# Kernel optimization log

Measured on AMD Instinct MI355X. Metric: run time of the kernel, lower is better.

The kernel has to match this reference:

```python
import jax, jax.numpy as jnp
import numpy as np

N_EXPERTS = 8
D_IN = 2048
D_OUT = 2048
BATCH = 8192


def setup_inputs() -> dict:
    key = jax.random.key(0)
    k_x, k_w, k_b, k_a, k_m = jax.random.split(key, 5)
    xs = jax.random.normal(k_x, (BATCH, D_IN), dtype=jnp.float32)
    # Expert parameters: each submodule modeled as Linear(D_IN, D_OUT)
    W = jax.random.normal(k_w, (N_EXPERTS, D_IN, D_OUT), dtype=jnp.float32) / np.sqrt(D_IN)
    b = jax.random.normal(k_b, (N_EXPERTS, D_OUT), dtype=jnp.float32) * 0.01
    actions = jax.random.randint(k_a, (BATCH,), 0, N_EXPERTS, dtype=jnp.int32)
    mxs = jax.random.randint(k_m, (BATCH,), 0, N_EXPERTS, dtype=jnp.int32)  # pass-through metadata
    return {"xs": xs, "W": W, "b": b, "mxs": mxs, "actions": actions}


def reference(xs, W, b, mxs, actions):
    # Original: per-sample split, route sample i to submodule actions[i], concat.
    # Vectorized MoE dispatch-combine: compute all expert outputs, select by one-hot.
    onehot = jax.nn.one_hot(actions, W.shape[0], dtype=xs.dtype)  # [B, E]
    # y_all[b,e,f] = xs[b,:] @ W[e,:,:]; combine with one-hot selection, add routed bias.
    ys = jnp.einsum('be,bd,edf->bf', onehot, xs, W) + b[actions]  # [B, D_OUT]
    return (ys, mxs, actions)
```

## Files before the change

### kernel.cpp

```cpp
#include <hip/hip_runtime.h>
#include <hip/hip_bf16.h>
#include <stdint.h>

#define BATCH 8192
#define GROWS 9216
#define DIN   2048
#define DOUT  2048
#define NEXP  8
#define BM    128
#define BN    256
#define BK    32
#define NT    (DIN / BK)
#define NSLOT 72
#define BUFSZ 24576
#define BOFF  8192

typedef __attribute__((ext_vector_type(4))) float fx4;
typedef __attribute__((ext_vector_type(8))) short sx8;

__device__ __forceinline__ short f2b(float x){
  unsigned u = __float_as_uint(x);
  u = u + 0x7FFFu + ((u >> 16) & 1u);
  return (short)(u >> 16);
}

__device__ __forceinline__ void gload16(const void* g, void* l){
  __builtin_amdgcn_global_load_lds(
      (const __attribute__((address_space(1))) unsigned int*)g,
      (__attribute__((address_space(3))) unsigned int*)l, 16, 0, 0);
}

__global__ void prep_count(const int* __restrict__ actions, int* __restrict__ perm,
                           int* __restrict__ meta){
  __shared__ int cnt[NEXP];
  int t = threadIdx.x;
  if (t < NEXP) cnt[t] = 0;
  for (int i = t; i < GROWS; i += 1024) perm[i] = -1;
  __syncthreads();
  for (int i = t; i < BATCH; i += 1024) atomicAdd(&cnt[actions[i]], 1);
  __syncthreads();
  if (t == 0){
    int s = 0, slot = 0;
    for (int e = 0; e < NEXP; ++e){
      meta[e] = s;
      int ns = (cnt[e] + BM - 1) / BM;
      for (int q = 0; q < ns; ++q) meta[17 + slot++] = e;
      s += ns * BM;
    }
    meta[16] = slot;
    meta[15] = 0;
  }
}

__global__ void prep_scatter(const int* __restrict__ actions, const int* __restrict__ mxs,
                             int* __restrict__ perm, int* __restrict__ meta,
                             float* __restrict__ out){
  int i = blockIdx.x * 256 + threadIdx.x;
  if (i < BATCH){
    int e = actions[i];
    int p = atomicAdd(&meta[e], 1);
    perm[p] = i;
    out[(size_t)BATCH * DOUT + i]         = (float)mxs[i];
    out[(size_t)BATCH * DOUT + BATCH + i] = (float)actions[i];
  }
}

__global__ void gatherx_kernel(const float* __restrict__ xs, const int* __restrict__ perm,
                               short* __restrict__ xp){
  int i = blockIdx.x;
  int t = threadIdx.x;
  short v[8];
  int p = perm[i];
  if (p >= 0){
    const fx4* src = (const fx4*)(xs + (size_t)p * DIN + t * 8);
    fx4 a = src[0], b2 = src[1];
    v[0]=f2b(a.x); v[1]=f2b(a.y); v[2]=f2b(a.z); v[3]=f2b(a.w);
    v[4]=f2b(b2.x); v[5]=f2b(b2.y); v[6]=f2b(b2.z); v[7]=f2b(b2.w);
  } else {
#pragma unroll
    for (int j = 0; j < 8; ++j) v[j] = 0;
  }
  *(sx8*)(xp + (size_t)i * DIN + t * 8) = *(const sx8*)v;
}

__global__ void transw_kernel(const float* __restrict__ W, short* __restrict__ Wt){
  __shared__ float tile[64][69];
  int e  = blockIdx.z;
  int n0 = blockIdx.x * 64;
  int k0 = blockIdx.y * 64;
  const float* Wp = W + (size_t)e * DIN * DOUT + (size_t)k0 * DOUT + n0;
  int t = threadIdx.x;
#pragma unroll
  for (int it = 0; it < 4; ++it){
    int r = it * 16 + (t >> 4);
    int c = (t & 15) * 4;
    fx4 v = *(const fx4*)(Wp + (size_t)r * DOUT + c);
    tile[r][c] = v.x; tile[r][c+1] = v.y; tile[r][c+2] = v.z; tile[r][c+3] = v.w;
  }
  __syncthreads();
  int n  = t >> 2;
  int kc = (t & 3) * 16;
  short vv[16];
#pragma unroll
  for (int j = 0; j < 16; ++j) vv[j] = f2b(tile[kc + j][n]);
  short* dst = Wt + (size_t)e * DOUT * DIN + (size_t)(n0 + n) * DIN + k0 + kc;
  *(sx8*)dst       = *(const sx8*)vv;
  *(sx8*)(dst + 8) = *(const sx8*)(vv + 8);
}

__global__ __launch_bounds__(512, 4)
void moe_gemm_kernel(const short* __restrict__ xp, const short* __restrict__ Wt,
                     const float* __restrict__ bias, const int* __restrict__ perm,
                     int* __restrict__ meta, float* __restrict__ out){
  __shared__ char lds[3 * BUFSZ];
  __shared__ int s_item;

  int nitems = meta[16] * 8;

  int t    = threadIdx.x;
  int wid  = t >> 6;
  int l    = t & 63;
  int wm   = wid & 1;
  int wn   = wid >> 1;
  int lrow = l & 15;
  int lk   = l >> 4;

  int srow = ((t >> 3) << 1) | ((t >> 2) & 1);
  int schk = (t & 3) ^ ((t >> 3) & 3);
  int ldst = t * 16;

  int arow = wm * 64 + lrow;
  int aline = arow >> 1;
  int addrA = aline * 128 + (arow & 1) * 64 + ((lk ^ (aline & 3)) << 4);
  int brow = wn * 64 + lrow;
  int bline = brow >> 1;
  int addrB = BOFF + bline * 128 + (brow & 1) * 64 + ((lk ^ (bline & 3)) << 4);

  for (;;){
    if (t == 0) s_item = atomicAdd(&meta[15], 1);
    __syncthreads();
    int item = s_item;
    if (item >= nitems) break;

    int slot = item >> 3, nb = item & 7;
    int e      = meta[17 + slot];
    int m_base = slot * BM;
    int n0     = nb * BN;

    const char* ag  = (const char*)xp + ((size_t)(m_base + srow) * DIN + schk * 8) * 2;
    const char* bg0 = (const char*)Wt + (((size_t)e * DOUT + n0 + srow) * DIN + schk * 8) * 2;
    const char* bg1 = bg0 + (size_t)128 * DIN * 2;

#define STAGE(kt, BASE) do{ \
    gload16(ag  + (size_t)(kt) * 64, lds + (BASE) + ldst); \
    gload16(bg0 + (size_t)(kt) * 64, lds + (BASE) + BOFF + ldst); \
    gload16(bg1 + (size_t)(kt) * 64, lds + (BASE) + BOFF + 8192 + ldst); \
  }while(0)

    fx4 acc[4][4];
#pragma unroll
    for (int m = 0; m < 4; ++m)
#pragma unroll
      for (int n = 0; n < 4; ++n)
        acc[m][n] = (fx4){0.f, 0.f, 0.f, 0.f};

    float bcol[4];
#pragma unroll
    for (int n = 0; n < 4; ++n)
      bcol[n] = bias[(size_t)e * DOUT + n0 + wn * 64 + n * 16 + lrow];

#define KSTEP(CB, SB, DOSTG, kt) do{ \
    sx8 af[4], bf[4]; \
    _Pragma("unroll") for (int m = 0; m < 4; ++m) \
      af[m] = *(const sx8*)(lds + (CB) + addrA + m * 1024); \
    _Pragma("unroll") for (int n = 0; n < 4; ++n) \
      bf[n] = *(const sx8*)(lds + (CB) + addrB + n * 1024); \
    if (DOSTG) STAGE((kt) + 2, SB); \
    __builtin_amdgcn_s_setprio(1); \
    _Pragma("unroll") for (int m = 0; m < 4; ++m) \
    _Pragma("unroll") for (int n = 0; n < 4; ++n) \
      acc[m][n] = __builtin_amdgcn_mfma_f32_16x16x32_bf16(af[m], bf[n], acc[m][n], 0, 0, 0); \
    __builtin_amdgcn_s_setprio(0); \
    if (DOSTG) asm volatile("s_waitcnt vmcnt(3)" ::: "memory"); \
    else       asm volatile("s_waitcnt vmcnt(0)" ::: "memory"); \
    __builtin_amdgcn_s_barrier(); \
    asm volatile("" ::: "memory"); \
  }while(0)

    STAGE(0, 0);
    STAGE(1, BUFSZ);
    asm volatile("s_waitcnt vmcnt(3)" ::: "memory");
    __builtin_amdgcn_s_barrier();
    asm volatile("" ::: "memory");

    for (int kt = 0; kt < 60; kt += 3){
      KSTEP(0,         2*BUFSZ, 1, kt);
      KSTEP(BUFSZ,     0,       1, kt + 1);
      KSTEP(2*BUFSZ,   BUFSZ,   1, kt + 2);
    }
    KSTEP(0,       2*BUFSZ, 1, 60);
    KSTEP(BUFSZ,   0,       1, 61);
    KSTEP(2*BUFSZ, 0,       0, 62);
    {
      sx8 af[4], bf[4];
#pragma unroll
      for (int m = 0; m < 4; ++m) af[m] = *(const sx8*)(lds + addrA + m * 1024);
#pragma unroll
      for (int n = 0; n < 4; ++n) bf[n] = *(const sx8*)(lds + addrB + n * 1024);
#pragma unroll
      for (int m = 0; m < 4; ++m)
#pragma unroll
        for (int n = 0; n < 4; ++n)
          acc[m][n] = __builtin_amdgcn_mfma_f32_16x16x32_bf16(af[m], bf[n], acc[m][n], 0, 0, 0);
    }

#pragma unroll
    for (int m = 0; m < 4; ++m){
      int rb = wm * 64 + m * 16 + lk * 4;
      int prow[4];
#pragma unroll
      for (int q = 0; q < 4; ++q)
        prow[q] = perm[m_base + rb + q];
#pragma unroll
      for (int n = 0; n < 4; ++n){
        int col = n0 + wn * 64 + n * 16 + lrow;
        fx4 v = acc[m][n];
#pragma unroll
        for (int q = 0; q < 4; ++q)
          if (prow[q] >= 0)
            out[(size_t)prow[q] * DOUT + col] = v[q] + bcol[n];
      }
    }
#undef KSTEP
#undef STAGE
  }
}

extern "C" void kernel_launch(void* const* d_in, const int* in_sizes, int n_in,
                              void* d_out, int out_size, void* d_ws, size_t ws_size,
                              hipStream_t stream) {
  const float* xs      = (const float*)d_in[0];
  const float* W       = (const float*)d_in[1];
  const float* b       = (const float*)d_in[2];
  const int*   mxs     = (const int*)d_in[3];
  const int*   actions = (const int*)d_in[4];
  float* out = (float*)d_out;

  int*   perm = (int*)d_ws;
  int*   meta = (int*)((char*)d_ws + 40960);
  short* Wt   = (short*)((char*)d_ws + 65536);
  short* xp   = (short*)((char*)d_ws + 65536 + (size_t)NEXP * DIN * DOUT * 2);

  hipLaunchKernelGGL(prep_count, dim3(1), dim3(1024), 0, stream, actions, perm, meta);
  hipLaunchKernelGGL(prep_scatter, dim3(32), dim3(256), 0, stream, actions, mxs, perm, meta, out);
  hipLaunchKernelGGL(gatherx_kernel, dim3(GROWS), dim3(256), 0, stream, xs, perm, xp);
  hipLaunchKernelGGL(transw_kernel, dim3(DOUT/64, DIN/64, NEXP), dim3(256), 0, stream, W, Wt);
  hipLaunchKernelGGL(moe_gemm_kernel, dim3(512), dim3(512), 0, stream,
                     xp, Wt, b, perm, meta, out);
}
```

Baseline: 209.9 us.

## Split expert rows into full 128-row tiles and thin 32-row remainder tiles

Expert segments are now padded to 32 rows instead of 128. Full 128-row tiles are assigned statically by block index, and the remainder tiles are processed by a new 32-row GEMM path that uses 4-byte LDS loads for A and a work-stealing queue. This cuts the MMA and load work wasted on padding rows and shrinks the gathered buffer. The routing-count kernel is also merged into the weight-transpose kernel as an extra block, which removes one launch. The thin path has lower MFMA density per B load, and with 512 blocks, leftover full tiles beyond the grid would never be computed.

```diff
diff --git a/kernel.cpp b/kernel.cpp
--- a/kernel.cpp
+++ b/kernel.cpp
@@ -3,15 +3,13 @@
 #include <stdint.h>
 
 #define BATCH 8192
-#define GROWS 9216
+#define GROWS 8448
 #define DIN   2048
 #define DOUT  2048
 #define NEXP  8
 #define BM    128
 #define BN    256
 #define BK    32
-#define NT    (DIN / BK)
-#define NSLOT 72
 #define BUFSZ 24576
 #define BOFF  8192
 
@@ -29,27 +27,59 @@
       (const __attribute__((address_space(1))) unsigned int*)g,
       (__attribute__((address_space(3))) unsigned int*)l, 16, 0, 0);
 }
-
-__global__ void prep_count(const int* __restrict__ actions, int* __restrict__ perm,
-                           int* __restrict__ meta){
-  __shared__ int cnt[NEXP];
+__device__ __forceinline__ void gload4(const void* g, void* l){
+  __builtin_amdgcn_global_load_lds(
+      (const __attribute__((address_space(1))) unsigned int*)g,
+      (__attribute__((address_space(3))) unsigned int*)l, 4, 0, 0);
+}
+
+__global__ void k1_kernel(const float* __restrict__ W, short* __restrict__ Wt,
+                          const int* __restrict__ actions, int* __restrict__ perm,
+                          int* __restrict__ meta){
+  __shared__ float tile[64][69];
   int t = threadIdx.x;
-  if (t < NEXP) cnt[t] = 0;
-  for (int i = t; i < GROWS; i += 1024) perm[i] = -1;
+  if (blockIdx.x == 8192){
+    int* cnt = (int*)tile;
+    if (t < NEXP) cnt[t] = 0;
+    for (int i = t; i < GROWS; i += 256) perm[i] = -1;
+    __syncthreads();
+    for (int i = t; i < BATCH; i += 256) atomicAdd(&cnt[actions[i]], 1);
+    __syncthreads();
+    if (t == 0){
+      int base = 0, fs = 0, ts = 0;
+      for (int e = 0; e < NEXP; ++e){
+        meta[e] = base;
+        int f = cnt[e] >> 7, rem = cnt[e] & 127;
+        for (int q = 0; q < f; ++q){ meta[16 + fs] = e; meta[80 + fs] = base; base += 128; ++fs; }
+        int th = (rem + 31) >> 5;
+        for (int q = 0; q < th; ++q){ meta[144 + ts] = e; meta[176 + ts] = base; base += 32; ++ts; }
+      }
+      meta[8] = fs * 8; meta[9] = ts * 8; meta[10] = 0;
+    }
+    return;
+  }
+  int id = blockIdx.x;
+  int e  = id >> 10;
+  int r2 = id & 1023;
+  int k0 = (r2 >> 5) << 6;
+  int n0 = (r2 & 31) << 6;
+  const float* Wp = W + (size_t)e * DIN * DOUT + (size_t)k0 * DOUT + n0;
+#pragma unroll
+  for (int it = 0; it < 4; ++it){
+    int r = it * 16 + (t >> 4);
+    int c = (t & 15) * 4;
+    fx4 v = *(const fx4*)(Wp + (size_t)r * DOUT + c);
+    tile[r][c] = v.x; tile[r][c+1] = v.y; tile[r][c+2] = v.z; tile[r][c+3] = v.w;
+  }
   __syncthreads();
-  for (int i = t; i < BATCH; i += 1024) atomicAdd(&cnt[actions[i]], 1);
-  __syncthreads();
-  if (t == 0){
-    int s = 0, slot = 0;
-    for (int e = 0; e < NEXP; ++e){
-      meta[e] = s;
-      int ns = (cnt[e] + BM - 1) / BM;
-      for (int q = 0; q < ns; ++q) meta[17 + slot++] = e;
-      s += ns * BM;
-    }
-    meta[16] = slot;
-    meta[15] = 0;
-  }
+  int n  = t >> 2;
+  int kc = (t & 3) * 16;
+  short vv[16];
+#pragma unroll
+  for (int j = 0; j < 16; ++j) vv[j] = f2b(tile[kc + j][n]);
+  short* dst = Wt + (size_t)e * DOUT * DIN + (size_t)(n0 + n) * DIN + k0 + kc;
+  *(sx8*)dst       = *(const sx8*)vv;
+  *(sx8*)(dst + 8) = *(const sx8*)(vv + 8);
 }
 
 __global__ void prep_scatter(const int* __restrict__ actions, const int* __restrict__ mxs,
@@ -83,39 +113,12 @@
   *(sx8*)(xp + (size_t)i * DIN + t * 8) = *(const sx8*)v;
 }
 
-__global__ void transw_kernel(const float* __restrict__ W, short* __restrict__ Wt){
-  __shared__ float tile[64][69];
-  int e  = blockIdx.z;
-  int n0 = blockIdx.x * 64;
-  int k0 = blockIdx.y * 64;
-  const float* Wp = W + (size_t)e * DIN * DOUT + (size_t)k0 * DOUT + n0;
-  int t = threadIdx.x;
-#pragma unroll
-  for (int it = 0; it < 4; ++it){
-    int r = it * 16 + (t >> 4);
-    int c = (t & 15) * 4;
-    fx4 v = *(const fx4*)(Wp + (size_t)r * DOUT + c);
-    tile[r][c] = v.x; tile[r][c+1] = v.y; tile[r][c+2] = v.z; tile[r][c+3] = v.w;
-  }
-  __syncthreads();
-  int n  = t >> 2;
-  int kc = (t & 3) * 16;
-  short vv[16];
-#pragma unroll
-  for (int j = 0; j < 16; ++j) vv[j] = f2b(tile[kc + j][n]);
-  short* dst = Wt + (size_t)e * DOUT * DIN + (size_t)(n0 + n) * DIN + k0 + kc;
-  *(sx8*)dst       = *(const sx8*)vv;
-  *(sx8*)(dst + 8) = *(const sx8*)(vv + 8);
-}
-
 __global__ __launch_bounds__(512, 4)
 void moe_gemm_kernel(const short* __restrict__ xp, const short* __restrict__ Wt,
                      const float* __restrict__ bias, const int* __restrict__ perm,
                      int* __restrict__ meta, float* __restrict__ out){
   __shared__ char lds[3 * BUFSZ];
   __shared__ int s_item;
-
-  int nitems = meta[16] * 8;
 
   int t    = threadIdx.x;
   int wid  = t >> 6;
@@ -128,7 +131,6 @@
   int srow = ((t >> 3) << 1) | ((t >> 2) & 1);
   int schk = (t & 3) ^ ((t >> 3) & 3);
   int ldst = t * 16;
-
   int arow = wm * 64 + lrow;
   int aline = arow >> 1;
   int addrA = aline * 128 + (arow & 1) * 64 + ((lk ^ (aline & 3)) << 4);
@@ -136,15 +138,13 @@
   int bline = brow >> 1;
   int addrB = BOFF + bline * 128 + (brow & 1) * 64 + ((lk ^ (bline & 3)) << 4);
 
-  for (;;){
-    if (t == 0) s_item = atomicAdd(&meta[15], 1);
-    __syncthreads();
-    int item = s_item;
-    if (item >= nitems) break;
-
-    int slot = item >> 3, nb = item & 7;
-    int e      = meta[17 + slot];
-    int m_base = slot * BM;
+  int nfull = meta[8], nthin = meta[9];
+  int F = blockIdx.x;
+
+  if (F < nfull){
+    int slot = F >> 3, nb = F & 7;
+    int e      = meta[16 + slot];
+    int m_base = meta[80 + slot];
     int n0     = nb * BN;
 
     const char* ag  = (const char*)xp + ((size_t)(m_base + srow) * DIN + schk * 8) * 2;
@@ -234,6 +234,100 @@
 #undef KSTEP
 #undef STAGE
   }
+
+  int wmT   = wid & 1;
+  int t_row = (t >> 2) & 31;
+  int t_off = (t >> 7) * 16 + (t & 3) * 4;
+  int addrAT = lk * 512 + (wmT * 16 + lrow) * 16;
+
+  for (;;){
+    if (t == 0) s_item = atomicAdd(&meta[10], 1);
+    __syncthreads();
+    int item = s_item;
+    if (item >= nthin) break;
+    int u = item >> 3, nb = item & 7;
+    int e      = meta[144 + u];
+    int m_base = meta[176 + u];
+    int n0     = nb * BN;
+
+    const char* agT = (const char*)xp + (size_t)(m_base + t_row) * (DIN * 2) + t_off;
+    const char* bg0 = (const char*)Wt + (((size_t)e * DOUT + n0 + srow) * DIN + schk * 8) * 2;
+    const char* bg1 = bg0 + (size_t)128 * DIN * 2;
+
+#define STAGET(kt, BASE) do{ \
+    gload4 (agT + (size_t)(kt) * 64, lds + (BASE) + t * 4); \
+    gload16(bg0 + (size_t)(kt) * 64, lds + (BASE) + BOFF + ldst); \
+    gload16(bg1 + (size_t)(kt) * 64, lds + (BASE) + BOFF + 8192 + ldst); \
+  }while(0)
+
+    fx4 accT[4];
+#pragma unroll
+    for (int n = 0; n < 4; ++n) accT[n] = (fx4){0.f, 0.f, 0.f, 0.f};
+
+    float bcol[4];
+#pragma unroll
+    for (int n = 0; n < 4; ++n)
+      bcol[n] = bias[(size_t)e * DOUT + n0 + wn * 64 + n * 16 + lrow];
+
+#define KSTEPT(CB, SB, DOSTG, kt) do{ \
+    sx8 af, bf[4]; \
+    af = *(const sx8*)(lds + (CB) + addrAT); \
+    _Pragma("unroll") for (int n = 0; n < 4; ++n) \
+      bf[n] = *(const sx8*)(lds + (CB) + addrB + n * 1024); \
+    if (DOSTG) STAGET((kt) + 2, SB); \
+    __builtin_amdgcn_s_setprio(1); \
+    _Pragma("unroll") for (int n = 0; n < 4; ++n) \
+      accT[n] = __builtin_amdgcn_mfma_f32_16x16x32_bf16(af, bf[n], accT[n], 0, 0, 0); \
+    __builtin_amdgcn_s_setprio(0); \
+    if (DOSTG) asm volatile("s_waitcnt vmcnt(3)" ::: "memory"); \
+    else       asm volatile("s_waitcnt vmcnt(0)" ::: "memory"); \
+    __builtin_amdgcn_s_barrier(); \
+    asm volatile("" ::: "memory"); \
+  }while(0)
+
+    STAGET(0, 0);
+    STAGET(1, BUFSZ);
+    asm volatile("s_waitcnt vmcnt(3)" ::: "memory");
+    __builtin_amdgcn_s_barrier();
+    asm volatile("" ::: "memory");
+
+    for (int kt = 0; kt < 60; kt += 3){
+      KSTEPT(0,         2*BUFSZ, 1, kt);
+      KSTEPT(BUFSZ,     0,       1, kt + 1);
+      KSTEPT(2*BUFSZ,   BUFSZ,   1, kt + 2);
+    }
+    KSTEPT(0,       2*BUFSZ, 1, 60);
+    KSTEPT(BUFSZ,   0,       1, 61);
+    KSTEPT(2*BUFSZ, 0,       0, 62);
+    {
+      sx8 af, bf[4];
+      af = *(const sx8*)(lds + addrAT);
+#pragma unroll
+      for (int n = 0; n < 4; ++n) bf[n] = *(const sx8*)(lds + addrB + n * 1024);
+#pragma unroll
+      for (int n = 0; n < 4; ++n)
+        accT[n] = __builtin_amdgcn_mfma_f32_16x16x32_bf16(af, bf[n], accT[n], 0, 0, 0);
+    }
+
+    {
+      int rb = wmT * 16 + lk * 4;
+      int prow[4];
+#pragma unroll
+      for (int q = 0; q < 4; ++q)
+        prow[q] = perm[m_base + rb + q];
+#pragma unroll
+      for (int n = 0; n < 4; ++n){
+        int col = n0 + wn * 64 + n * 16 + lrow;
+        fx4 v = accT[n];
+#pragma unroll
+        for (int q = 0; q < 4; ++q)
+          if (prow[q] >= 0)
+            out[(size_t)prow[q] * DOUT + col] = v[q] + bcol[n];
+      }
+    }
+#undef KSTEPT
+#undef STAGET
+  }
 }
 
 extern "C" void kernel_launch(void* const* d_in, const int* in_sizes, int n_in,
@@ -251,10 +345,9 @@
   short* Wt   = (short*)((char*)d_ws + 65536);
   short* xp   = (short*)((char*)d_ws + 65536 + (size_t)NEXP * DIN * DOUT * 2);
 
-  hipLaunchKernelGGL(prep_count, dim3(1), dim3(1024), 0, stream, actions, perm, meta);
+  hipLaunchKernelGGL(k1_kernel, dim3(8193), dim3(256), 0, stream, W, Wt, actions, perm, meta);
   hipLaunchKernelGGL(prep_scatter, dim3(32), dim3(256), 0, stream, actions, mxs, perm, meta, out);
   hipLaunchKernelGGL(gatherx_kernel, dim3(GROWS), dim3(256), 0, stream, xs, perm, xp);
-  hipLaunchKernelGGL(transw_kernel, dim3(DOUT/64, DIN/64, NEXP), dim3(256), 0, stream, W, Wt);
   hipLaunchKernelGGL(moe_gemm_kernel, dim3(512), dim3(512), 0, stream,
                      xp, Wt, b, perm, meta, out);
 }
```

Result: no change. 213.1 us (+1.5%).

## Split-K tail slots, static GEMM grid, and merge prep/transform kernels

Applied to the files above, without the earlier changes.

Replaces the persistent atomic work-queue GEMM with a static grid where the first 64 slots run full-K tiles and slots beyond 64 are split into two K halves writing bf16 partials to a workspace buffer, reduced by a new kernel that adds bias. It also fuses prep_count and prep_scatter into one single-block kernel and merges the x gather and W transpose into one launch. The aim is to balance the wave tail over the 256 CUs and cut launch count. The trade-offs are bf16 rounding of partial sums, extra traffic and a launch for the reduction, and a serial single-block scatter.

```diff
diff --git a/kernel.cpp b/kernel.cpp
--- a/kernel.cpp
+++ b/kernel.cpp
@@ -10,8 +10,6 @@
 #define BM    128
 #define BN    256
 #define BK    32
-#define NT    (DIN / BK)
-#define NSLOT 72
 #define BUFSZ 24576
 #define BOFF  8192
 
@@ -23,6 +21,9 @@
   u = u + 0x7FFFu + ((u >> 16) & 1u);
   return (short)(u >> 16);
 }
+__device__ __forceinline__ float b2f(short v){
+  return __uint_as_float(((unsigned)(unsigned short)v) << 16);
+}
 
 __device__ __forceinline__ void gload16(const void* g, void* l){
   __builtin_amdgcn_global_load_lds(
@@ -30,8 +31,9 @@
       (__attribute__((address_space(3))) unsigned int*)l, 16, 0, 0);
 }
 
-__global__ void prep_count(const int* __restrict__ actions, int* __restrict__ perm,
-                           int* __restrict__ meta){
+__global__ void prep_kernel(const int* __restrict__ actions, const int* __restrict__ mxs,
+                            int* __restrict__ perm, int* __restrict__ meta,
+                            float* __restrict__ out){
   __shared__ int cnt[NEXP];
   int t = threadIdx.x;
   if (t < NEXP) cnt[t] = 0;
@@ -48,15 +50,9 @@
       s += ns * BM;
     }
     meta[16] = slot;
-    meta[15] = 0;
-  }
-}
-
-__global__ void prep_scatter(const int* __restrict__ actions, const int* __restrict__ mxs,
-                             int* __restrict__ perm, int* __restrict__ meta,
-                             float* __restrict__ out){
-  int i = blockIdx.x * 256 + threadIdx.x;
-  if (i < BATCH){
+  }
+  __syncthreads();
+  for (int i = t; i < BATCH; i += 1024){
     int e = actions[i];
     int p = atomicAdd(&meta[e], 1);
     perm[p] = i;
@@ -65,31 +61,33 @@
   }
 }
 
-__global__ void gatherx_kernel(const float* __restrict__ xs, const int* __restrict__ perm,
-                               short* __restrict__ xp){
-  int i = blockIdx.x;
+__global__ void k2_kernel(const float* __restrict__ W, short* __restrict__ Wt,
+                          const float* __restrict__ xs, const int* __restrict__ perm,
+                          short* __restrict__ xp){
+  __shared__ float tile[64][69];
   int t = threadIdx.x;
-  short v[8];
-  int p = perm[i];
-  if (p >= 0){
-    const fx4* src = (const fx4*)(xs + (size_t)p * DIN + t * 8);
-    fx4 a = src[0], b2 = src[1];
-    v[0]=f2b(a.x); v[1]=f2b(a.y); v[2]=f2b(a.z); v[3]=f2b(a.w);
-    v[4]=f2b(b2.x); v[5]=f2b(b2.y); v[6]=f2b(b2.z); v[7]=f2b(b2.w);
-  } else {
-#pragma unroll
-    for (int j = 0; j < 8; ++j) v[j] = 0;
-  }
-  *(sx8*)(xp + (size_t)i * DIN + t * 8) = *(const sx8*)v;
-}
-
-__global__ void transw_kernel(const float* __restrict__ W, short* __restrict__ Wt){
-  __shared__ float tile[64][69];
-  int e  = blockIdx.z;
-  int n0 = blockIdx.x * 64;
-  int k0 = blockIdx.y * 64;
+  if (blockIdx.x >= 8192){
+    int i = blockIdx.x - 8192;
+    short v[8];
+    int p = perm[i];
+    if (p >= 0){
+      const fx4* src = (const fx4*)(xs + (size_t)p * DIN + t * 8);
+      fx4 a = src[0], b2 = src[1];
+      v[0]=f2b(a.x); v[1]=f2b(a.y); v[2]=f2b(a.z); v[3]=f2b(a.w);
+      v[4]=f2b(b2.x); v[5]=f2b(b2.y); v[6]=f2b(b2.z); v[7]=f2b(b2.w);
+    } else {
+#pragma unroll
+      for (int j = 0; j < 8; ++j) v[j] = 0;
+    }
+    *(sx8*)(xp + (size_t)i * DIN + t * 8) = *(const sx8*)v;
+    return;
+  }
+  int id = blockIdx.x;
+  int e  = id >> 10;
+  int r2 = id & 1023;
+  int k0 = (r2 >> 5) << 6;
+  int n0 = (r2 & 31) << 6;
   const float* Wp = W + (size_t)e * DIN * DOUT + (size_t)k0 * DOUT + n0;
-  int t = threadIdx.x;
 #pragma unroll
   for (int it = 0; it < 4; ++it){
     int r = it * 16 + (t >> 4);
@@ -111,11 +109,21 @@
 __global__ __launch_bounds__(512, 4)
 void moe_gemm_kernel(const short* __restrict__ xp, const short* __restrict__ Wt,
                      const float* __restrict__ bias, const int* __restrict__ perm,
-                     int* __restrict__ meta, float* __restrict__ out){
+                     const int* __restrict__ meta, float* __restrict__ out,
+                     short* __restrict__ tailbuf){
   __shared__ char lds[3 * BUFSZ];
-  __shared__ int s_item;
-
-  int nitems = meta[16] * 8;
+
+  int nslots = meta[16];
+  int F = blockIdx.x;
+  int slot, nb, z = 0, h = 0, k0 = 0;
+  bool tail = (F >= 512);
+  if (!tail){ slot = F >> 3; nb = F & 7; }
+  else { int j = F - 512; z = j >> 4; int rem = j & 15; nb = rem >> 1; h = rem & 1;
+         slot = 64 + z; k0 = h * 32; }
+  if (slot >= nslots) return;
+  int e      = meta[17 + slot];
+  int m_base = slot * BM;
+  int n0     = nb * BN;
 
   int t    = threadIdx.x;
   int wid  = t >> 6;
@@ -128,6 +136,9 @@
   int srow = ((t >> 3) << 1) | ((t >> 2) & 1);
   int schk = (t & 3) ^ ((t >> 3) & 3);
   int ldst = t * 16;
+  const char* ag  = (const char*)xp + ((size_t)(m_base + srow) * DIN + schk * 8) * 2;
+  const char* bg0 = (const char*)Wt + (((size_t)e * DOUT + n0 + srow) * DIN + schk * 8) * 2;
+  const char* bg1 = bg0 + (size_t)128 * DIN * 2;
 
   int arow = wm * 64 + lrow;
   int aline = arow >> 1;
@@ -136,38 +147,18 @@
   int bline = brow >> 1;
   int addrB = BOFF + bline * 128 + (brow & 1) * 64 + ((lk ^ (bline & 3)) << 4);
 
-  for (;;){
-    if (t == 0) s_item = atomicAdd(&meta[15], 1);
-    __syncthreads();
-    int item = s_item;
-    if (item >= nitems) break;
-
-    int slot = item >> 3, nb = item & 7;
-    int e      = meta[17 + slot];
-    int m_base = slot * BM;
-    int n0     = nb * BN;
-
-    const char* ag  = (const char*)xp + ((size_t)(m_base + srow) * DIN + schk * 8) * 2;
-    const char* bg0 = (const char*)Wt + (((size_t)e * DOUT + n0 + srow) * DIN + schk * 8) * 2;
-    const char* bg1 = bg0 + (size_t)128 * DIN * 2;
+  fx4 acc[4][4];
+#pragma unroll
+  for (int m = 0; m < 4; ++m)
+#pragma unroll
+    for (int n = 0; n < 4; ++n)
+      acc[m][n] = (fx4){0.f, 0.f, 0.f, 0.f};
 
 #define STAGE(kt, BASE) do{ \
     gload16(ag  + (size_t)(kt) * 64, lds + (BASE) + ldst); \
     gload16(bg0 + (size_t)(kt) * 64, lds + (BASE) + BOFF + ldst); \
     gload16(bg1 + (size_t)(kt) * 64, lds + (BASE) + BOFF + 8192 + ldst); \
   }while(0)
-
-    fx4 acc[4][4];
-#pragma unroll
-    for (int m = 0; m < 4; ++m)
-#pragma unroll
-      for (int n = 0; n < 4; ++n)
-        acc[m][n] = (fx4){0.f, 0.f, 0.f, 0.f};
-
-    float bcol[4];
-#pragma unroll
-    for (int n = 0; n < 4; ++n)
-      bcol[n] = bias[(size_t)e * DOUT + n0 + wn * 64 + n * 16 + lrow];
 
 #define KSTEP(CB, SB, DOSTG, kt) do{ \
     sx8 af[4], bf[4]; \
@@ -187,11 +178,17 @@
     asm volatile("" ::: "memory"); \
   }while(0)
 
-    STAGE(0, 0);
-    STAGE(1, BUFSZ);
-    asm volatile("s_waitcnt vmcnt(3)" ::: "memory");
-    __builtin_amdgcn_s_barrier();
-    asm volatile("" ::: "memory");
+  STAGE(k0, 0);
+  STAGE(k0 + 1, BUFSZ);
+  asm volatile("s_waitcnt vmcnt(3)" ::: "memory");
+  __builtin_amdgcn_s_barrier();
+  asm volatile("" ::: "memory");
+
+  if (!tail){
+    float bcol[4];
+#pragma unroll
+    for (int n = 0; n < 4; ++n)
+      bcol[n] = bias[(size_t)e * DOUT + n0 + wn * 64 + n * 16 + lrow];
 
     for (int kt = 0; kt < 60; kt += 3){
       KSTEP(0,         2*BUFSZ, 1, kt);
@@ -213,7 +210,6 @@
         for (int n = 0; n < 4; ++n)
           acc[m][n] = __builtin_amdgcn_mfma_f32_16x16x32_bf16(af[m], bf[n], acc[m][n], 0, 0, 0);
     }
-
 #pragma unroll
     for (int m = 0; m < 4; ++m){
       int rb = wm * 64 + m * 16 + lk * 4;
@@ -231,9 +227,66 @@
             out[(size_t)prow[q] * DOUT + col] = v[q] + bcol[n];
       }
     }
+  } else {
+    for (int i = 0; i < 30; i += 3){
+      KSTEP(0,         2*BUFSZ, 1, k0 + i);
+      KSTEP(BUFSZ,     0,       1, k0 + i + 1);
+      KSTEP(2*BUFSZ,   BUFSZ,   1, k0 + i + 2);
+    }
+    KSTEP(0, 0, 0, k0 + 30);
+    {
+      sx8 af[4], bf[4];
+#pragma unroll
+      for (int m = 0; m < 4; ++m) af[m] = *(const sx8*)(lds + BUFSZ + addrA + m * 1024);
+#pragma unroll
+      for (int n = 0; n < 4; ++n) bf[n] = *(const sx8*)(lds + BUFSZ + addrB + n * 1024);
+#pragma unroll
+      for (int m = 0; m < 4; ++m)
+#pragma unroll
+        for (int n = 0; n < 4; ++n)
+          acc[m][n] = __builtin_amdgcn_mfma_f32_16x16x32_bf16(af[m], bf[n], acc[m][n], 0, 0, 0);
+    }
+    short* base = tailbuf + ((size_t)(h * 8 + z) * 128) * DOUT;
+#pragma unroll
+    for (int m = 0; m < 4; ++m){
+      int rb = wm * 64 + m * 16 + lk * 4;
+#pragma unroll
+      for (int n = 0; n < 4; ++n){
+        int col = n0 + wn * 64 + n * 16 + lrow;
+        fx4 v = acc[m][n];
+#pragma unroll
+        for (int q = 0; q < 4; ++q)
+          base[(size_t)(rb + q) * DOUT + col] = f2b(v[q]);
+      }
+    }
+  }
 #undef KSTEP
 #undef STAGE
-  }
+}
+
+__global__ void reduce_kernel(const short* __restrict__ tailbuf, const float* __restrict__ bias,
+                              const int* __restrict__ perm, const int* __restrict__ meta,
+                              float* __restrict__ out){
+  int nslots = meta[16];
+  int blk = blockIdx.x;
+  int z = blk >> 7, r = blk & 127;
+  int slot = 64 + z;
+  if (slot >= nslots) return;
+  int p = perm[slot * BM + r];
+  if (p < 0) return;
+  int e = meta[17 + slot];
+  int c = threadIdx.x * 8;
+  const short* h0 = tailbuf + ((size_t)(z)     * 128 + r) * DOUT + c;
+  const short* h1 = tailbuf + ((size_t)(8 + z) * 128 + r) * DOUT + c;
+  sx8 a = *(const sx8*)h0;
+  sx8 b = *(const sx8*)h1;
+  const float* bs = bias + (size_t)e * DOUT + c;
+  float o[8];
+#pragma unroll
+  for (int j = 0; j < 8; ++j) o[j] = b2f(a[j]) + b2f(b[j]) + bs[j];
+  float* dst = out + (size_t)p * DOUT + c;
+  *(fx4*)dst       = *(const fx4*)o;
+  *(fx4*)(dst + 4) = *(const fx4*)(o + 4);
 }
 
 extern "C" void kernel_launch(void* const* d_in, const int* in_sizes, int n_in,
@@ -250,11 +303,11 @@
   int*   meta = (int*)((char*)d_ws + 40960);
   short* Wt   = (short*)((char*)d_ws + 65536);
   short* xp   = (short*)((char*)d_ws + 65536 + (size_t)NEXP * DIN * DOUT * 2);
-
-  hipLaunchKernelGGL(prep_count, dim3(1), dim3(1024), 0, stream, actions, perm, meta);
-  hipLaunchKernelGGL(prep_scatter, dim3(32), dim3(256), 0, stream, actions, mxs, perm, meta, out);
-  hipLaunchKernelGGL(gatherx_kernel, dim3(GROWS), dim3(256), 0, stream, xs, perm, xp);
-  hipLaunchKernelGGL(transw_kernel, dim3(DOUT/64, DIN/64, NEXP), dim3(256), 0, stream, W, Wt);
-  hipLaunchKernelGGL(moe_gemm_kernel, dim3(512), dim3(512), 0, stream,
-                     xp, Wt, b, perm, meta, out);
-}
+  short* tailbuf = (short*)((char*)xp + (size_t)GROWS * DIN * 2);
+
+  hipLaunchKernelGGL(prep_kernel, dim3(1), dim3(1024), 0, stream, actions, mxs, perm, meta, out);
+  hipLaunchKernelGGL(k2_kernel, dim3(8192 + GROWS), dim3(256), 0, stream, W, Wt, xs, perm, xp);
+  hipLaunchKernelGGL(moe_gemm_kernel, dim3(640), dim3(512), 0, stream,
+                     xp, Wt, b, perm, meta, out, tailbuf);
+  hipLaunchKernelGGL(reduce_kernel, dim3(1024), dim3(256), 0, stream, tailbuf, b, perm, meta, out);
+}
```

After: 188.4 us. 1.11x faster.
